# Performance work log

Measured on AMD Instinct MI355X. Metric: run time of the kernel, lower is better.

## Reference

```python
import jax
import jax.numpy as jnp
import numpy as np
from jax.scipy.linalg import expm

H = 2048   # hidden_size
R = 1      # low-rank dimension
B = 2048   # batch of independent (h, x) pairs


def _glorot(key, shape):
    return jax.random.uniform(key, shape, minval=-1.0, maxval=1.0) * jnp.sqrt(2.0 / sum(shape))


def setup_inputs() -> dict:
    key = jax.random.key(0)
    k1, k2, k3, k4, k5, k6 = jax.random.split(key, 6)
    return {
        "h": jax.random.normal(k5, (B, H), dtype=jnp.float32),
        "x": jax.random.normal(k6, (B, H), dtype=jnp.float32),
        # a_diag ~ U(-1, 0) * init_scale (10.0): negative real diagonal
        "a_diag": jax.random.uniform(k1, (H,), minval=-1.0, maxval=0.0) * 10.0,
        "p_vec": _glorot(k2, (H, R)),
        "q_vec": _glorot(k3, (H, R)),
        "b_mat": _glorot(k4, (H, H)),
        "delta": jnp.array(0.1, dtype=jnp.float32),
    }


def reference(h, x, a_diag, p_vec, q_vec, b_mat, delta):
    # A = diag(a_diag) + P Q^T  (DPLR structure, materialized dense as in source)
    A = jnp.diag(a_diag) + p_vec @ q_vec.T                       # [H, H]
    # Discretized state matrix: exp(delta * A)
    expA = expm(delta * A)                                       # [H, H]
    # Discretized input matrix: A^{-1} (exp(delta A) - I) B  (pinv as in source)
    A_inv = jnp.linalg.pinv(A)                                   # [H, H]
    B_disc = A_inv @ (expA - jnp.eye(H, dtype=A.dtype)) @ b_mat  # [H, H]
    # Batched recurrence step: A h + B x  for each row of h, x
    return h @ expA.T + x @ B_disc.T                             # [B, H]
```

## Files before the change

kernel.cpp:

```cpp
#include <hip/hip_runtime.h>

#define MAXM 16
#define NL_CAP 256
#define THETA 0.02f
#define SMEM_BYTES 32768

typedef unsigned short u16;
typedef u16 u16x8 __attribute__((ext_vector_type(8)));
typedef u16 u16x4 __attribute__((ext_vector_type(4)));
typedef __bf16 bf16x8 __attribute__((ext_vector_type(8)));
typedef float f32x4 __attribute__((ext_vector_type(4)));


__device__ __forceinline__ u16 f2bf(float f) {
    unsigned u = __float_as_uint(f);
    return (u16)((u + 0x7fffu + ((u >> 16) & 1u)) >> 16);
}

__global__ __launch_bounds__(256)
void conv_k(const float* __restrict__ x, const float* __restrict__ b,
            u16* __restrict__ xb, u16* __restrict__ bb, long nx, long nb)
{
    long i = ((long)blockIdx.x * 256 + threadIdx.x) * 4;
    if (i < nx) {
        float4 v = *(const float4*)&x[i];
        u16x4 o = {f2bf(v.x), f2bf(v.y), f2bf(v.z), f2bf(v.w)};
        *(u16x4*)&xb[i] = o;
    }
    if (i < nb) {
        float4 v = *(const float4*)&b[i];
        u16x4 o = {f2bf(v.x), f2bf(v.y), f2bf(v.z), f2bf(v.w)};
        *(u16x4*)&bb[i] = o;
    }
}


__device__ __forceinline__ double frcp(double den) {
    double r = (double)__builtin_amdgcn_rcpf((float)den);
    return fma(r, fma(-den, r, 1.0), r);
}


__device__ __forceinline__ void gload_lds16(const void* g, void* l) {
    __builtin_amdgcn_global_load_lds(
        (const __attribute__((address_space(1))) unsigned int*)g,
        (__attribute__((address_space(3))) unsigned int*)l, 16, 0, 0);
}

__device__ __forceinline__ void gemm_tile(u16* Al, u16* Bl, int tid, int bx, int by,
                                          const u16* __restrict__ A,
                                          const u16* __restrict__ B,
                                          float* __restrict__ C,
                                          int Ndim, int Kstride, int Klen)
{
    const int bm = by * 128, bn = bx * 128;
    const int wv = tid >> 6, ln = tid & 63;
    const int wr = (wv >> 1) * 64, wc = (wv & 1) * 64;
    const int fr = ln & 15, fk = (ln >> 4) * 8;
    const int fk2 = fk ^ ((fr & 3) << 3);

    const int r0 = tid >> 2;
    const int c0 = ((tid & 3) ^ (r0 & 3)) * 8;
    const u16* Ap0 = A + (size_t)(bm + r0) * Kstride + c0;
    const u16* Ap1 = Ap0 + (size_t)64 * Kstride;
    const u16* Bp0 = B + (size_t)(bn + r0) * Kstride + c0;
    const u16* Bp1 = Bp0 + (size_t)64 * Kstride;

    f32x4 acc[4][4];
#pragma unroll
    for (int m = 0; m < 4; ++m)
#pragma unroll
        for (int n = 0; n < 4; ++n) acc[m][n] = (f32x4)0.f;

    {
        u16* a0 = Al + wv * 512;
        u16* a1 = Al + 2048 + wv * 512;
        u16* b0 = Bl + wv * 512;
        u16* b1 = Bl + 2048 + wv * 512;
        gload_lds16(Ap0, a0);
        gload_lds16(Ap1, a1);
        gload_lds16(Bp0, b0);
        gload_lds16(Bp1, b1);
    }

    int cur = 0;
    for (int kk = 0; kk < Klen; kk += 32) {
        const bool hasNext = (kk + 32 < Klen);
        if (hasNext) {
            const int nb = (cur ^ 1) * 4096;
            u16* a0 = Al + nb + wv * 512;
            u16* a1 = Al + nb + 2048 + wv * 512;
            u16* b0 = Bl + nb + wv * 512;
            u16* b1 = Bl + nb + 2048 + wv * 512;
            gload_lds16(Ap0 + kk + 32, a0);
            gload_lds16(Ap1 + kk + 32, a1);
            gload_lds16(Bp0 + kk + 32, b0);
            gload_lds16(Bp1 + kk + 32, b1);
            asm volatile("s_waitcnt vmcnt(4)" ::: "memory");
        } else {
            asm volatile("s_waitcnt vmcnt(0)" ::: "memory");
        }
        __builtin_amdgcn_sched_barrier(0);
        __builtin_amdgcn_s_barrier();

        const int cb = cur * 4096;
        u16x8 af[4], bf[4];
#pragma unroll
        for (int m = 0; m < 4; ++m)
            af[m] = *(const u16x8*)&Al[cb + (wr + m * 16 + fr) * 32 + fk2];
#pragma unroll
        for (int n = 0; n < 4; ++n)
            bf[n] = *(const u16x8*)&Bl[cb + (wc + n * 16 + fr) * 32 + fk2];
#pragma unroll
        for (int m = 0; m < 4; ++m)
#pragma unroll
            for (int n = 0; n < 4; ++n)
                acc[m][n] = __builtin_amdgcn_mfma_f32_16x16x32_bf16(
                    __builtin_bit_cast(bf16x8, af[m]),
                    __builtin_bit_cast(bf16x8, bf[n]), acc[m][n], 0, 0, 0);

        __builtin_amdgcn_sched_barrier(0);
        __builtin_amdgcn_s_barrier();
        cur ^= 1;
    }

    const int crow = (ln >> 4) * 4;
#pragma unroll
    for (int m = 0; m < 4; ++m)
#pragma unroll
        for (int n = 0; n < 4; ++n) {
            const size_t base = (size_t)(bm + wr + m * 16 + crow) * Ndim
                              + bn + wc + n * 16 + fr;
#pragma unroll
            for (int j = 0; j < 4; ++j)
                C[base + (size_t)j * Ndim] = acc[m][n][j];
        }
}

__global__ __launch_bounds__(256)
void bgemm_k(const u16* __restrict__ A, const u16* __restrict__ B,
             float* __restrict__ C, int Ndim, int Kdim)
{
    __shared__ __align__(16) unsigned char smem[SMEM_BYTES];
    gemm_tile((u16*)smem, (u16*)smem + 8192, threadIdx.x,
              blockIdx.x, blockIdx.y, A, B, C, Ndim, Kdim, Kdim);
}


__global__ __launch_bounds__(256)
void g_sgemm_k(const float* __restrict__ A, const float* __restrict__ B,
               float* __restrict__ C, int Mdim, int Ndim, int Kdim)
{
    __shared__ __align__(16) float As[16][132];
    __shared__ __align__(16) float Bs[16][68];
    const int tid = threadIdx.x;
    const int tx = tid & 15, ty = tid >> 4;
    const int bn = blockIdx.x * 64, bm = blockIdx.y * 128;
    const int lrA = tid >> 1, lcA = (tid & 1) << 3;
    const int lrB = tid >> 2, lcB = (tid & 3) << 2;
    const float* Aptr = A + (size_t)(bm + lrA) * Kdim + lcA;
    const float* Bptr = B + (size_t)(bn + lrB) * Kdim + lcB;
    float4 a0 = *(const float4*)(Aptr);
    float4 a1 = *(const float4*)(Aptr + 4);
    float4 b0 = *(const float4*)(Bptr);
    float acc[8][4];
#pragma unroll
    for (int i = 0; i < 8; ++i)
#pragma unroll
        for (int j = 0; j < 4; ++j) acc[i][j] = 0.f;
    for (int kk = 0; kk < Kdim; kk += 16) {
        __syncthreads();
        As[lcA + 0][lrA] = a0.x; As[lcA + 1][lrA] = a0.y;
        As[lcA + 2][lrA] = a0.z; As[lcA + 3][lrA] = a0.w;
        As[lcA + 4][lrA] = a1.x; As[lcA + 5][lrA] = a1.y;
        As[lcA + 6][lrA] = a1.z; As[lcA + 7][lrA] = a1.w;
        Bs[lcB + 0][lrB] = b0.x; Bs[lcB + 1][lrB] = b0.y;
        Bs[lcB + 2][lrB] = b0.z; Bs[lcB + 3][lrB] = b0.w;
        __syncthreads();
        if (kk + 16 < Kdim) {
            a0 = *(const float4*)(Aptr + kk + 16);
            a1 = *(const float4*)(Aptr + kk + 20);
            b0 = *(const float4*)(Bptr + kk + 16);
        }
#pragma unroll
        for (int k = 0; k < 16; ++k) {
            const float4 av0 = *(const float4*)&As[k][ty * 8];
            const float4 av1 = *(const float4*)&As[k][ty * 8 + 4];
            const float4 bv  = *(const float4*)&Bs[k][tx * 4];
            const float avf[8] = {av0.x, av0.y, av0.z, av0.w, av1.x, av1.y, av1.z, av1.w};
            const float bvf[4] = {bv.x, bv.y, bv.z, bv.w};
#pragma unroll
            for (int i = 0; i < 8; ++i)
#pragma unroll
                for (int j = 0; j < 4; ++j) acc[i][j] += avf[i] * bvf[j];
        }
    }
#pragma unroll
    for (int i = 0; i < 8; ++i) {
        const int r = bm + ty * 8 + i;
        float4 v = {acc[i][0], acc[i][1], acc[i][2], acc[i][3]};
        *(float4*)&C[(size_t)r * Ndim + bn + tx * 4] = v;
    }
}


__device__ __forceinline__ double wsum(double x) {
#pragma unroll
    for (int m = 32; m; m >>= 1) x += __shfl_xor(x, m, 64);
    return x;
}
__device__ __forceinline__ float wsumf(float x) {
#pragma unroll
    for (int m = 32; m; m >>= 1) x += __shfl_xor(x, m, 64);
    return x;
}

__device__ __forceinline__ int inert(double s11, double s12, double s22,
                                     double dc, double cS)
{
    double b00 = cS - s11, b01 = -1.0 - s12, b11 = -s22;
    double det = b00 * b11 - b01 * b01, tr = b00 + b11;
    int neg = (det > 0.0) ? ((tr < 0.0) ? 2 : 0) : 1;
    return (int)(dc + 0.5) + neg - 1;
}

__device__ __forceinline__ int lane_evalN32(float tf, double td, int n4,
    const float4* l0, const float4* l1, const float4* l2,
    const double* pc, bool poly, double cS,
    double& g11o, double& g12o, double& g22o)
{
    float s11 = 0.f, s12 = 0.f, s22 = 0.f, dc = 0.f;
#pragma unroll 4
    for (int i = 0; i < n4; ++i) {
        const float4 d4 = l0[i], x4 = l1[i], y4 = l2[i];
        const float dd[4] = {d4.x, d4.y, d4.z, d4.w};
        const float xx[4] = {x4.x, x4.y, x4.z, x4.w};
        const float yy[4] = {y4.x, y4.y, y4.z, y4.w};
#pragma unroll
        for (int e = 0; e < 4; ++e) {
            float den = dd[e] - tf;
            float mag = fmaxf(fabsf(den), 1e-30f);
            den = (den < 0.f) ? -mag : mag;
            const float inv = __builtin_amdgcn_rcpf(den);
            s11 = fmaf(xx[e] * xx[e], inv, s11);
            s12 = fmaf(xx[e] * yy[e], inv, s12);
            s22 = fmaf(yy[e] * yy[e], inv, s22);
            if (dd[e] < tf) dc += 1.f;
        }
    }
    double S11 = (double)s11, S12 = (double)s12, S22 = (double)s22;
    if (poly) {
        S11 += pc[0] + td * (pc[3] + td * (pc[6] + td * pc[9]));
        S12 += pc[1] + td * (pc[4] + td * (pc[7] + td * pc[10]));
        S22 += pc[2] + td * (pc[5] + td * (pc[8] + td * pc[11]));
    }
    g11o = S11; g12o = S12; g22o = S22;
    return inert(S11, S12, S22, (double)dc, cS);
}

__device__ void spec256(unsigned char* smem, int tid,
                        const float* __restrict__ av, const float* __restrict__ pv,
                        const float* __restrict__ qv, double* __restrict__ hdr,
                        float* __restrict__ V)
{
    __builtin_amdgcn_s_setprio(1);

    float* sd2 = (float*)smem;
    float* sw1 = sd2 + 2048;
    float* sw2 = sw1 + 2048;
    float* nl0 = sw2 + 2048;
    float* nl1 = nl0 + NL_CAP;
    float* nl2 = nl1 + NL_CAP;
    double* dsh = (double*)(nl2 + NL_CAP);
    int* ish = (int*)(dsh + 192);

    const int lane = tid & 63, wv = tid >> 6;
    const int j0 = tid * 8;

    float d2r[8], w1r[8], w2r[8];
    double cS = 0, n1 = 0, n2 = 0, mx = 0;
#pragma unroll
    for (int h = 0; h < 2; ++h) {
        float4 aa = *(const float4*)&av[j0 + h * 4];
        float4 pp = *(const float4*)&pv[j0 + h * 4];
        float4 qq = *(const float4*)&qv[j0 + h * 4];
        const float a4[4] = {aa.x, aa.y, aa.z, aa.w};
        const float p4[4] = {pp.x, pp.y, pp.z, pp.w};
        const float q4[4] = {qq.x, qq.y, qq.z, qq.w};
#pragma unroll
        for (int e = 0; e < 4; ++e) {
            const int ix = h * 4 + e;
            d2r[ix] = a4[e] * a4[e];
            w1r[ix] = a4[e] * p4[e];
            w2r[ix] = q4[e];
            sd2[j0 + ix] = d2r[ix]; sw1[j0 + ix] = w1r[ix]; sw2[j0 + ix] = w2r[ix];
            cS += (double)p4[e] * p4[e];
            n1 += (double)w1r[ix] * w1r[ix];
            n2 += (double)w2r[ix] * w2r[ix];
            mx = fmax(mx, (double)d2r[ix]);
        }
    }
    cS = wsum(cS); n1 = wsum(n1); n2 = wsum(n2);
#pragma unroll
    for (int m_ = 32; m_; m_ >>= 1) mx = fmax(mx, __shfl_xor(mx, m_, 64));
    __syncthreads();
    if (lane == 0) { dsh[wv] = cS; dsh[4 + wv] = n1; dsh[8 + wv] = n2; dsh[12 + wv] = mx; }
    __syncthreads();
    cS = 0; n1 = 0; n2 = 0; mx = 0;
    for (int w = 0; w < 4; ++w) {
        cS += dsh[w]; n1 += dsh[4 + w]; n2 += dsh[8 + w];
        mx = fmax(mx, dsh[12 + w]);
    }
    __syncthreads();

    const double pert = 2.0 * sqrt(n1 * n2) + cS * n2;
    double lo = fmax(0.0, mx - pert);
    double hi = mx + pert + 0.5;
    for (int r = 0; r < 3; ++r) {
        const double td = lo + (hi - lo) * (double)(wv + 1) / 5.0;
        const float tf = (float)td;
        float s11 = 0.f, s12 = 0.f, s22 = 0.f, dc = 0.f;
        for (int i4 = lane; i4 < 512; i4 += 64) {
            const float4 dd = ((const float4*)sd2)[i4];
            const float4 e1 = ((const float4*)sw1)[i4];
            const float4 e2 = ((const float4*)sw2)[i4];
            const float df[4] = {dd.x, dd.y, dd.z, dd.w};
            const float f1[4] = {e1.x, e1.y, e1.z, e1.w};
            const float f2[4] = {e2.x, e2.y, e2.z, e2.w};
#pragma unroll
            for (int e = 0; e < 4; ++e) {
                float den = df[e] - tf;
                float mag = fmaxf(fabsf(den), 1e-30f);
                den = (den < 0.f) ? -mag : mag;
                const float inv = __builtin_amdgcn_rcpf(den);
                s11 = fmaf(f1[e] * f1[e], inv, s11);
                s12 = fmaf(f1[e] * f2[e], inv, s12);
                s22 = fmaf(f2[e] * f2[e], inv, s22);
                if (df[e] < tf) dc += 1.f;
            }
        }
        s11 = wsumf(s11); s12 = wsumf(s12); s22 = wsumf(s22); dc = wsumf(dc);
        if (lane == 0)
            ish[wv] = inert((double)s11, (double)s12, (double)s22, (double)dc, cS);
        __syncthreads();
        double nlo = lo, nhi = hi;
        for (int i = 0; i < 4; ++i) {
            double ti = lo + (hi - lo) * (double)(i + 1) / 5.0;
            if (ish[i] >= 2048) { if (ti < nhi) nhi = ti; }
            else                { if (ti > nlo) nlo = ti; }
        }
        lo = nlo; hi = nhi;
        __syncthreads();
    }
    const double lmax = 0.5 * (lo + hi);
    const double rc = 10.0 * 2048.0 * 1.1920928955078125e-07;
    const double cut2 = rc * rc * lmax;

    int flags = 0, lc = 0;
#pragma unroll
    for (int e = 0; e < 8; ++e)
        if (d2r[e] < THETA) { flags |= (1 << e); ++lc; }
    int sc = lc;
#pragma unroll
    for (int off = 1; off < 64; off <<= 1) {
        int y = __shfl_up(sc, off, 64);
        if (lane >= off) sc += y;
    }
    const int wtot = __shfl(sc, 63, 64);
    const int excl = sc - lc;
    if (lane == 0) ish[4 + wv] = wtot;
    __syncthreads();
    int base = excl;
    for (int w = 0; w < wv; ++w) base += ish[4 + w];
    int cnt = 0;
    for (int w = 0; w < 4; ++w) cnt += ish[4 + w];
    {
        int pos = base;
#pragma unroll
        for (int e = 0; e < 8; ++e) {
            if (flags & (1 << e)) {
                if (pos < NL_CAP) { nl0[pos] = d2r[e]; nl1[pos] = w1r[e]; nl2[pos] = w2r[e]; }
                ++pos;
            }
        }
    }
    const int cntPad = (cnt + 7) & ~7;
    if (tid == 0) {
        for (int i = cnt; i < cntPad && i < NL_CAP; ++i) {
            nl0[i] = 1e30f; nl1[i] = 0.f; nl2[i] = 0.f;
        }
        ish[8] = cnt; ish[10] = cntPad >> 2;
    }

    float cff[12];
#pragma unroll
    for (int c = 0; c < 12; ++c) cff[c] = 0.f;
#pragma unroll
    for (int e = 0; e < 8; ++e) {
        if (d2r[e] >= THETA) {
            float id = __builtin_amdgcn_rcpf(d2r[e]);
            float b1 = w1r[e], b2 = w2r[e];
            float x11 = b1 * b1, x12 = b1 * b2, x22 = b2 * b2;
            float f = id;
            cff[0] += x11 * f; cff[1]  += x12 * f; cff[2]  += x22 * f; f *= id;
            cff[3] += x11 * f; cff[4]  += x12 * f; cff[5]  += x22 * f; f *= id;
            cff[6] += x11 * f; cff[7]  += x12 * f; cff[8]  += x22 * f; f *= id;
            cff[9] += x11 * f; cff[10] += x12 * f; cff[11] += x22 * f;
        }
    }
#pragma unroll
    for (int c = 0; c < 12; ++c) cff[c] = wsumf(cff[c]);
    if (lane == 0) {
        double* dw = &dsh[16 + wv * 12];
#pragma unroll
        for (int c = 0; c < 12; ++c) dw[c] = (double)cff[c];
    }
    __syncthreads();
    if (tid < 12) {
        double s = 0;
        for (int w = 0; w < 4; ++w) s += dsh[16 + w * 12 + tid];
        dsh[96 + tid] = s;
    }
    __syncthreads();

    cnt = ish[8];
    const bool nearOK = (cnt <= NL_CAP - 8);
    const float4* l0 = nearOK ? (const float4*)nl0 : (const float4*)sd2;
    const float4* l1 = nearOK ? (const float4*)nl1 : (const float4*)sw1;
    const float4* l2 = nearOK ? (const float4*)nl2 : (const float4*)sw2;
    const int n4 = nearOK ? ish[10] : 512;
    const bool poly = nearOK;
    const double* pcoef = &dsh[96];

    double zg1, zg2, zg3;
    if (wv == 0) {
        int N = lane_evalN32((float)cut2, cut2, n4, l0, l1, l2, pcoef, poly, cS,
                             zg1, zg2, zg3);
        if (lane == 0) ish[9] = N;
    }
    __syncthreads();
    int m = ish[9];
    if (m < 0) m = 0;
    if (m > MAXM) m = MAXM;

    for (int k = wv; k < m; k += 4) {
        double klo = 0.0, khi = cut2;
        for (int r = 0; r < 2; ++r) {
            const double w = khi - klo;
            const double td = klo + w * (double)(lane + 1) / 65.0;
            int N = lane_evalN32((float)td, td, n4, l0, l1, l2, pcoef, poly, cS,
                                 zg1, zg2, zg3);
            unsigned long long mask = __ballot(N >= k + 1);
            int j = (mask == 0ull) ? 64 : (__ffsll(mask) - 1);
            double nk = (j == 64) ? khi : (klo + w * (double)(j + 1) / 65.0);
            klo = klo + w * (double)j / 65.0;
            khi = nk;
        }
        const double lam = 0.5 * (klo + khi);
        double g11, g12, g22;
        lane_evalN32((float)lam, lam, n4, l0, l1, l2, pcoef, poly, cS, g11, g12, g22);
        const double m00 = 1.0 + g12, m01 = g11 + cS * g12;
        const double m10 = g22,       m11 = 1.0 + g12 + cS * g22;
        double y1, y2;
        if (m00 * m00 + m01 * m01 >= m10 * m10 + m11 * m11) { y1 = m01; y2 = -m00; }
        else                                                { y1 = m11; y2 = -m10; }
        double z1 = y2, z2 = y1 + cS * y2;
        const double zs = 1.0 / fmax(fmax(fabs(z1), fabs(z2)), 1e-300);
        if (lane == 0) {
            dsh[112 + 3 * k]     = lam;
            dsh[112 + 3 * k + 1] = z1 * zs;
            dsh[112 + 3 * k + 2] = z2 * zs;
        }
    }
    __syncthreads();

    for (int k = 0; k < m; ++k) {
        const double lam = dsh[112 + 3 * k];
        const float z1 = (float)dsh[112 + 3 * k + 1];
        const float z2 = (float)dsh[112 + 3 * k + 2];
        float vr[8];
        float pn = 0.f;
#pragma unroll
        for (int e = 0; e < 8; ++e) {
            const double dend = (double)d2r[e] - lam;
            float den = (float)dend;
            float mag = fmaxf(fabsf(den), 1e-12f);
            den = (den < 0.f) ? -mag : mag;
            const float vi = (w1r[e] * z1 + w2r[e] * z2) * __builtin_amdgcn_rcpf(den);
            pn = fmaf(vi, vi, pn);
            vr[e] = vi;
        }
        pn = wsumf(pn);
        if (lane == 0) dsh[160 + wv] = (double)pn;
        __syncthreads();
        double tot = 0;
        for (int w = 0; w < 4; ++w) tot += dsh[160 + w];
        const float inv = (float)(1.0 / sqrt(tot));
        float o0[8];
#pragma unroll
        for (int e = 0; e < 8; ++e) o0[e] = vr[e] * inv;
        *(float4*)&V[(size_t)k * 2048 + j0]     = *(float4*)&o0[0];
        *(float4*)&V[(size_t)k * 2048 + j0 + 4] = *(float4*)&o0[4];
        __syncthreads();
    }

    if (tid == 0) { hdr[0] = lmax; hdr[1] = cut2; hdr[2] = (double)m; hdr[3] = cS; }
    __builtin_amdgcn_s_setprio(0);
}


__global__ __launch_bounds__(256)
void fat_k(const u16* __restrict__ A, const u16* __restrict__ B,
           float* __restrict__ C0, float* __restrict__ C1,
           int Ndim, int Kdim, int ntiles, int nbx, int nsplit,
           const float* __restrict__ av, const float* __restrict__ pv,
           const float* __restrict__ qv, double* __restrict__ hdr,
           float* __restrict__ V)
{
    __shared__ __align__(16) unsigned char smem[SMEM_BYTES];
    const int bid = blockIdx.x;
    if (bid == 0) {
        spec256(smem, threadIdx.x, av, pv, qv, hdr, V);
        return;
    }
    if ((bid & 255) == 0) return;
    const int t = bid - 1 - (bid >> 8);
    if (t >= ntiles * nsplit) return;
    const int ks = t / ntiles;
    const int tt = t - ks * ntiles;
    const int Klen = Kdim / nsplit;
    gemm_tile((u16*)smem, (u16*)smem + 8192, threadIdx.x,
              tt % nbx, tt / nbx,
              A + (size_t)ks * Klen, B + (size_t)ks * Klen,
              ks ? C1 : C0, Ndim, Kdim, Klen);
}


__global__ __launch_bounds__(256, 2)
void series_k(float* __restrict__ io, const float* __restrict__ io2, int addP,
              const float* __restrict__ hm,
              const float* __restrict__ qv, const float* __restrict__ pv,
              const float* __restrict__ av, const float* __restrict__ delta,
              const float* __restrict__ V, const double* __restrict__ hdr,
              int useTrunc)
{
    const int lane = threadIdx.x & 63;
    const int row = blockIdx.x * 4 + (threadIdx.x >> 6);
    const float d = delta[0];
    const int m = useTrunc ? (int)hdr[2] : 0;

    float q[32], p[32], a[32], t[32], o[32];
    float* iorow = io + (size_t)row * 2048;
    const float* io2row = io2 + (size_t)row * 2048;
#pragma unroll
    for (int cc = 0; cc < 8; ++cc) {
        const int j = cc * 256 + lane * 4;
        *(float4*)&q[cc * 4] = *(const float4*)&qv[j];
        *(float4*)&p[cc * 4] = *(const float4*)&pv[j];
        *(float4*)&a[cc * 4] = *(const float4*)&av[j];
        float4 u0 = *(const float4*)&iorow[j];
        if (addP) {
            const float4 u1 = *(const float4*)&io2row[j];
            u0.x += u1.x; u0.y += u1.y; u0.z += u1.z; u0.w += u1.w;
        }
        *(float4*)&t[cc * 4] = u0;
    }
#pragma unroll
    for (int e = 0; e < 32; ++e) o[e] = t[e];

    float cf = 1.f;
    for (int k = 1; k <= 13; ++k) {
        float s = 0.f;
#pragma unroll
        for (int e = 0; e < 32; ++e) s += t[e] * q[e];
#pragma unroll
        for (int msk = 32; msk; msk >>= 1) s += __shfl_xor(s, msk, 64);
        cf /= (float)(k + 1);
        const float ds = d * s;
#pragma unroll
        for (int e = 0; e < 32; ++e) { t[e] = d * a[e] * t[e] + ds * p[e]; o[e] += cf * t[e]; }
    }
#pragma unroll
    for (int e = 0; e < 32; ++e) o[e] *= d;

    for (int k = 0; k < m; ++k) {
        const float* vr = V + (size_t)k * 2048;
        float vk[32];
#pragma unroll
        for (int cc = 0; cc < 8; ++cc)
            *(float4*)&vk[cc * 4] = *(const float4*)&vr[cc * 256 + lane * 4];
        float s = 0.f;
#pragma unroll
        for (int e = 0; e < 32; ++e) s += o[e] * vk[e];
#pragma unroll
        for (int msk = 32; msk; msk >>= 1) s += __shfl_xor(s, msk, 64);
#pragma unroll
        for (int e = 0; e < 32; ++e) o[e] -= s * vk[e];
    }

    const float* hrow = hm + (size_t)row * 2048;
#pragma unroll
    for (int cc = 0; cc < 8; ++cc)
        *(float4*)&t[cc * 4] = *(const float4*)&hrow[cc * 256 + lane * 4];
#pragma unroll
    for (int e = 0; e < 32; ++e) o[e] += t[e];
    cf = 1.f;
    for (int k = 1; k <= 14; ++k) {
        float s = 0.f;
#pragma unroll
        for (int e = 0; e < 32; ++e) s += t[e] * q[e];
#pragma unroll
        for (int msk = 32; msk; msk >>= 1) s += __shfl_xor(s, msk, 64);
        cf /= (float)k;
        const float ds = d * s;
#pragma unroll
        for (int e = 0; e < 32; ++e) { t[e] = d * a[e] * t[e] + ds * p[e]; o[e] += cf * t[e]; }
    }
#pragma unroll
    for (int cc = 0; cc < 8; ++cc)
        *(float4*)&iorow[cc * 256 + lane * 4] = *(const float4*)&o[cc * 4];
}


extern "C" void kernel_launch(void* const* d_in, const int* in_sizes, int n_in,
                              void* d_out, int out_size, void* d_ws, size_t ws_size,
                              hipStream_t stream)
{
    const float* hmat  = (const float*)d_in[0];
    const float* xmat  = (const float*)d_in[1];
    const float* adiag = (const float*)d_in[2];
    const float* pvec  = (const float*)d_in[3];
    const float* qvec  = (const float*)d_in[4];
    const float* bmat  = (const float*)d_in[5];
    const float* delta = (const float*)d_in[6];
    float* out = (float*)d_out;

    const int H  = in_sizes[2];
    const int Bb = in_sizes[0] / H;
    const size_t SZ = (size_t)Bb * H;
    const size_t HH = (size_t)H * H;

    double* hdr = (double*)d_ws;
    float* V = (float*)(hdr + 8);
    u16* xb = (u16*)(V + (size_t)MAXM * H);
    u16* bb = xb + SZ;
    float* C1 = (float*)(bb + HH);

    const size_t needSpec  = 64 + (size_t)MAXM * H * sizeof(float);
    const size_t needFull  = needSpec + (SZ + HH) * sizeof(u16);
    const size_t needSplit = needFull + SZ * sizeof(float);
    const bool doTrunc = (H == 2048) && (ws_size >= needSpec);
    const bool doBf16  = (ws_size >= needFull) && (H % 128 == 0) && (Bb % 128 == 0);
    const bool doSplit = doBf16 && doTrunc && (ws_size >= needSplit);

    dim3 blk256(256);
    const int nbx = H / 128;
    const int ntiles = nbx * (Bb / 128);

    if (doBf16) {
        const long nmax = (long)(SZ > HH ? SZ : HH);
        const int cg = (int)((nmax / 4 + 255) / 256);
        conv_k<<<cg, blk256, 0, stream>>>(xmat, bmat, xb, bb, (long)SZ, (long)HH);
        if (doTrunc) {
            const int nsplit = doSplit ? 2 : 1;
            const int NT = ntiles * nsplit;
            const int grid = 1 + NT + (NT + 254) / 255;
            fat_k<<<grid, blk256, 0, stream>>>(
                xb, bb, out, C1, H, H, ntiles, nbx, nsplit,
                adiag, pvec, qvec, hdr, V);
        } else {
            dim3 gg(nbx, Bb / 128);
            bgemm_k<<<gg, blk256, 0, stream>>>(xb, bb, out, H, H);
        }
    } else {
        if (doTrunc)
            fat_k<<<1, blk256, 0, stream>>>(nullptr, nullptr, out, nullptr,
                                            H, H, 0, 1, 1,
                                            adiag, pvec, qvec, hdr, V);
        dim3 gg(H / 64, Bb / 128);
        g_sgemm_k<<<gg, blk256, 0, stream>>>(xmat, bmat, out, Bb, H, H);
    }

    series_k<<<Bb / 4, blk256, 0, stream>>>(out, doSplit ? C1 : out,
                                            doSplit ? 1 : 0,
                                            hmat, qvec, pvec, adiag, delta,
                                            V, hdr, doTrunc ? 1 : 0);
}
```

Before: 77.13 us.

## Fuse fp32-to-bf16 conversion into GEMM tile loads and drop conv kernel

Removes the separate conversion kernel that wrote bf16 copies of x and b_mat to workspace. The GEMM tile now loads fp32 straight from global memory into registers, packs pairs with v_cvt_pk_bf16_f32, and stores them into single-buffered LDS, prefetching the next K slice into registers while the MFMAs run. This saves one launch and a full read/write pass over about 16M elements, but each tile reads twice the bytes from global memory and gives up the async global_load_lds double buffering.

After: 84.33 us. 1.09x slower.

```diff
diff --git a/kernel.cpp b/kernel.cpp
--- a/kernel.cpp
+++ b/kernel.cpp
@@ -4,34 +4,24 @@
 #define NL_CAP 256
 #define THETA 0.02f
 #define SMEM_BYTES 32768
+#define GSMEM 16384
 
 typedef unsigned short u16;
 typedef u16 u16x8 __attribute__((ext_vector_type(8)));
-typedef u16 u16x4 __attribute__((ext_vector_type(4)));
 typedef __bf16 bf16x8 __attribute__((ext_vector_type(8)));
 typedef float f32x4 __attribute__((ext_vector_type(4)));
 
 
-__device__ __forceinline__ u16 f2bf(float f) {
-    unsigned u = __float_as_uint(f);
-    return (u16)((u + 0x7fffu + ((u >> 16) & 1u)) >> 16);
-}
-
-__global__ __launch_bounds__(256)
-void conv_k(const float* __restrict__ x, const float* __restrict__ b,
-            u16* __restrict__ xb, u16* __restrict__ bb, long nx, long nb)
-{
-    long i = ((long)blockIdx.x * 256 + threadIdx.x) * 4;
-    if (i < nx) {
-        float4 v = *(const float4*)&x[i];
-        u16x4 o = {f2bf(v.x), f2bf(v.y), f2bf(v.z), f2bf(v.w)};
-        *(u16x4*)&xb[i] = o;
-    }
-    if (i < nb) {
-        float4 v = *(const float4*)&b[i];
-        u16x4 o = {f2bf(v.x), f2bf(v.y), f2bf(v.z), f2bf(v.w)};
-        *(u16x4*)&bb[i] = o;
-    }
+__device__ __forceinline__ unsigned pk2(float lo, float hi) {
+    unsigned r;
+    asm("v_cvt_pk_bf16_f32 %0, %1, %2" : "=v"(r) : "v"(lo), "v"(hi));
+    return r;
+}
+__device__ __forceinline__ uint4 pk8(float4 a, float4 b) {
+    uint4 r;
+    r.x = pk2(a.x, a.y); r.y = pk2(a.z, a.w);
+    r.z = pk2(b.x, b.y); r.w = pk2(b.z, b.w);
+    return r;
 }
 
 
@@ -41,15 +31,9 @@
 }
 
 
-__device__ __forceinline__ void gload_lds16(const void* g, void* l) {
-    __builtin_amdgcn_global_load_lds(
-        (const __attribute__((address_space(1))) unsigned int*)g,
-        (__attribute__((address_space(3))) unsigned int*)l, 16, 0, 0);
-}
-
 __device__ __forceinline__ void gemm_tile(u16* Al, u16* Bl, int tid, int bx, int by,
-                                          const u16* __restrict__ A,
-                                          const u16* __restrict__ B,
+                                          const float* __restrict__ A,
+                                          const float* __restrict__ B,
                                           float* __restrict__ C,
                                           int Ndim, int Kstride, int Klen)
 {
@@ -60,11 +44,16 @@
     const int fk2 = fk ^ ((fr & 3) << 3);
 
     const int r0 = tid >> 2;
-    const int c0 = ((tid & 3) ^ (r0 & 3)) * 8;
-    const u16* Ap0 = A + (size_t)(bm + r0) * Kstride + c0;
-    const u16* Ap1 = Ap0 + (size_t)64 * Kstride;
-    const u16* Bp0 = B + (size_t)(bn + r0) * Kstride + c0;
-    const u16* Bp1 = Bp0 + (size_t)64 * Kstride;
+    const int cc = tid & 3;
+    const int dst = ((cc ^ (r0 & 3)) << 3);
+    const float* Ap0 = A + (size_t)(bm + r0) * Kstride + cc * 8;
+    const float* Ap1 = Ap0 + (size_t)64 * Kstride;
+    const float* Bp0 = B + (size_t)(bn + r0) * Kstride + cc * 8;
+    const float* Bp1 = Bp0 + (size_t)64 * Kstride;
+    uint4* Ad0 = (uint4*)&Al[r0 * 32 + dst];
+    uint4* Ad1 = (uint4*)&Al[(r0 + 64) * 32 + dst];
+    uint4* Bd0 = (uint4*)&Bl[r0 * 32 + dst];
+    uint4* Bd1 = (uint4*)&Bl[(r0 + 64) * 32 + dst];
 
     f32x4 acc[4][4];
 #pragma unroll
@@ -72,45 +61,30 @@
 #pragma unroll
         for (int n = 0; n < 4; ++n) acc[m][n] = (f32x4)0.f;
 
-    {
-        u16* a0 = Al + wv * 512;
-        u16* a1 = Al + 2048 + wv * 512;
-        u16* b0 = Bl + wv * 512;
-        u16* b1 = Bl + 2048 + wv * 512;
-        gload_lds16(Ap0, a0);
-        gload_lds16(Ap1, a1);
-        gload_lds16(Bp0, b0);
-        gload_lds16(Bp1, b1);
-    }
-
-    int cur = 0;
+    float4 ra0a, ra0b, ra1a, ra1b, rb0a, rb0b, rb1a, rb1b;
+#define LOAD8(ko) {                                                     \
+    ra0a = *(const float4*)(Ap0 + (ko)); ra0b = *(const float4*)(Ap0 + (ko) + 4); \
+    ra1a = *(const float4*)(Ap1 + (ko)); ra1b = *(const float4*)(Ap1 + (ko) + 4); \
+    rb0a = *(const float4*)(Bp0 + (ko)); rb0b = *(const float4*)(Bp0 + (ko) + 4); \
+    rb1a = *(const float4*)(Bp1 + (ko)); rb1b = *(const float4*)(Bp1 + (ko) + 4); }
+
+    LOAD8(0);
+
     for (int kk = 0; kk < Klen; kk += 32) {
-        const bool hasNext = (kk + 32 < Klen);
-        if (hasNext) {
-            const int nb = (cur ^ 1) * 4096;
-            u16* a0 = Al + nb + wv * 512;
-            u16* a1 = Al + nb + 2048 + wv * 512;
-            u16* b0 = Bl + nb + wv * 512;
-            u16* b1 = Bl + nb + 2048 + wv * 512;
-            gload_lds16(Ap0 + kk + 32, a0);
-            gload_lds16(Ap1 + kk + 32, a1);
-            gload_lds16(Bp0 + kk + 32, b0);
-            gload_lds16(Bp1 + kk + 32, b1);
-            asm volatile("s_waitcnt vmcnt(4)" ::: "memory");
-        } else {
-            asm volatile("s_waitcnt vmcnt(0)" ::: "memory");
-        }
-        __builtin_amdgcn_sched_barrier(0);
-        __builtin_amdgcn_s_barrier();
-
-        const int cb = cur * 4096;
+        *Ad0 = pk8(ra0a, ra0b);
+        *Ad1 = pk8(ra1a, ra1b);
+        *Bd0 = pk8(rb0a, rb0b);
+        *Bd1 = pk8(rb1a, rb1b);
+        __syncthreads();
+        if (kk + 32 < Klen) LOAD8(kk + 32);
+
         u16x8 af[4], bf[4];
 #pragma unroll
         for (int m = 0; m < 4; ++m)
-            af[m] = *(const u16x8*)&Al[cb + (wr + m * 16 + fr) * 32 + fk2];
+            af[m] = *(const u16x8*)&Al[(wr + m * 16 + fr) * 32 + fk2];
 #pragma unroll
         for (int n = 0; n < 4; ++n)
-            bf[n] = *(const u16x8*)&Bl[cb + (wc + n * 16 + fr) * 32 + fk2];
+            bf[n] = *(const u16x8*)&Bl[(wc + n * 16 + fr) * 32 + fk2];
 #pragma unroll
         for (int m = 0; m < 4; ++m)
 #pragma unroll
@@ -121,8 +95,8 @@
 
         __builtin_amdgcn_sched_barrier(0);
         __builtin_amdgcn_s_barrier();
-        cur ^= 1;
-    }
+    }
+#undef LOAD8
 
     const int crow = (ln >> 4) * 4;
 #pragma unroll
@@ -135,15 +109,6 @@
             for (int j = 0; j < 4; ++j)
                 C[base + (size_t)j * Ndim] = acc[m][n][j];
         }
-}
-
-__global__ __launch_bounds__(256)
-void bgemm_k(const u16* __restrict__ A, const u16* __restrict__ B,
-             float* __restrict__ C, int Ndim, int Kdim)
-{
-    __shared__ __align__(16) unsigned char smem[SMEM_BYTES];
-    gemm_tile((u16*)smem, (u16*)smem + 8192, threadIdx.x,
-              blockIdx.x, blockIdx.y, A, B, C, Ndim, Kdim, Kdim);
 }
 
 
@@ -510,7 +475,7 @@
 
 
 __global__ __launch_bounds__(256)
-void fat_k(const u16* __restrict__ A, const u16* __restrict__ B,
+void fat_k(const float* __restrict__ A, const float* __restrict__ B,
            float* __restrict__ C0, float* __restrict__ C1,
            int Ndim, int Kdim, int ntiles, int nbx, int nsplit,
            const float* __restrict__ av, const float* __restrict__ pv,
@@ -529,7 +494,7 @@
     const int ks = t / ntiles;
     const int tt = t - ks * ntiles;
     const int Klen = Kdim / nsplit;
-    gemm_tile((u16*)smem, (u16*)smem + 8192, threadIdx.x,
+    gemm_tile((u16*)smem, (u16*)smem + 4096, threadIdx.x,
               tt % nbx, tt / nbx,
               A + (size_t)ks * Klen, B + (size_t)ks * Klen,
               ks ? C1 : C0, Ndim, Kdim, Klen);
@@ -638,40 +603,28 @@
     const int H  = in_sizes[2];
     const int Bb = in_sizes[0] / H;
     const size_t SZ = (size_t)Bb * H;
-    const size_t HH = (size_t)H * H;
 
     double* hdr = (double*)d_ws;
-    float* V = (float*)(hdr + 8);
-    u16* xb = (u16*)(V + (size_t)MAXM * H);
-    u16* bb = xb + SZ;
-    float* C1 = (float*)(bb + HH);
+    float* V  = (float*)(hdr + 8);
+    float* C1 = V + (size_t)MAXM * H;
 
     const size_t needSpec  = 64 + (size_t)MAXM * H * sizeof(float);
-    const size_t needFull  = needSpec + (SZ + HH) * sizeof(u16);
-    const size_t needSplit = needFull + SZ * sizeof(float);
+    const size_t needSplit = needSpec + SZ * sizeof(float);
     const bool doTrunc = (H == 2048) && (ws_size >= needSpec);
-    const bool doBf16  = (ws_size >= needFull) && (H % 128 == 0) && (Bb % 128 == 0);
-    const bool doSplit = doBf16 && doTrunc && (ws_size >= needSplit);
+    const bool doMFMA  = (H % 128 == 0) && (Bb % 128 == 0);
+    const bool doSplit = doMFMA && doTrunc && (ws_size >= needSplit);
 
     dim3 blk256(256);
     const int nbx = H / 128;
     const int ntiles = nbx * (Bb / 128);
 
-    if (doBf16) {
-        const long nmax = (long)(SZ > HH ? SZ : HH);
-        const int cg = (int)((nmax / 4 + 255) / 256);
-        conv_k<<<cg, blk256, 0, stream>>>(xmat, bmat, xb, bb, (long)SZ, (long)HH);
-        if (doTrunc) {
-            const int nsplit = doSplit ? 2 : 1;
-            const int NT = ntiles * nsplit;
-            const int grid = 1 + NT + (NT + 254) / 255;
-            fat_k<<<grid, blk256, 0, stream>>>(
-                xb, bb, out, C1, H, H, ntiles, nbx, nsplit,
-                adiag, pvec, qvec, hdr, V);
-        } else {
-            dim3 gg(nbx, Bb / 128);
-            bgemm_k<<<gg, blk256, 0, stream>>>(xb, bb, out, H, H);
-        }
+    if (doTrunc && doMFMA) {
+        const int nsplit = doSplit ? 2 : 1;
+        const int NT = ntiles * nsplit;
+        const int grid = 1 + NT + (NT + 254) / 255;
+        fat_k<<<grid, blk256, 0, stream>>>(
+            xmat, bmat, out, C1, H, H, ntiles, nbx, nsplit,
+            adiag, pvec, qvec, hdr, V);
     } else {
         if (doTrunc)
             fat_k<<<1, blk256, 0, stream>>>(nullptr, nullptr, out, nullptr,
```
